# Performance work log

Hardware: AMD Instinct MI355X
Metric: run time of the kernel (lower is better)

## Reference

```python
import jax, jax.numpy as jnp
import numpy as np


def _prelu(x, a):
    return jnp.where(x >= 0, x, a * x)


def _conv1x1(x, w, b, a):
    # x: (B,C,H,W), w: (O,C), b: (O,), a: PReLU scalar (shared, torch default)
    y = jnp.einsum('bchw,oc->bohw', x, w) + b[None, :, None, None]
    return _prelu(y, a)


def setup_inputs() -> dict:
    key = jax.random.key(0)
    ks = jax.random.split(key, 7)
    B, C, H, W = 8, 128, 256, 256
    std = 1.0 / np.sqrt(C)
    x = jax.random.normal(ks[0], (B, C, H, W), dtype=jnp.float32)
    Wf = jax.random.normal(ks[1], (C, C), dtype=jnp.float32) * std
    bf = jax.random.normal(ks[2], (C,), dtype=jnp.float32) * std
    Wg = jax.random.normal(ks[3], (C, C), dtype=jnp.float32) * std
    bg = jax.random.normal(ks[4], (C,), dtype=jnp.float32) * std
    Wh = jax.random.normal(ks[5], (C, C), dtype=jnp.float32) * std
    bh = jax.random.normal(ks[6], (C,), dtype=jnp.float32) * std
    af = jnp.float32(0.25)
    ag = jnp.float32(0.25)
    ah = jnp.float32(0.25)
    return {"x": x, "Wf": Wf, "bf": bf, "af": af,
            "Wg": Wg, "bg": bg, "ag": ag,
            "Wh": Wh, "bh": bh, "ah": ah}


def reference(x, Wf, bf, af, Wg, bg, ag, Wh, bh, ah):
    # 1x1 conv projections + PReLU
    map_f = _conv1x1(x, Wf, bf, af)          # (B,C,H,W)
    map_g = _conv1x1(x, Wg, bg, ag)          # (B,C,H,W)
    map_h = _conv1x1(x, Wh, bh, ah)          # (B,C,H,W)
    # map_f.transpose(2,3) @ map_g -> (B,C,W,W), unscaled single-head attention
    atten = jnp.einsum('bchw,bchv->bcwv', map_f, map_g)  # (B,C,W,W)
    atten = jax.nn.softmax(atten, axis=-1)
    # map_h @ atten -> (B,C,H,W)
    out = jnp.einsum('bchw,bcwv->bchv', map_h, atten)
    return out + x
```

## Files before the change

### kernel.cpp

```cpp
#include <hip/hip_runtime.h>

typedef __bf16 bf16_t;
typedef __bf16 bf16x8 __attribute__((ext_vector_type(8)));
typedef __bf16 bf16x4 __attribute__((ext_vector_type(4)));
typedef float  f32x4  __attribute__((ext_vector_type(4)));

#define HW_ 65536
#define C_  128

__device__ __forceinline__ int swz(int r) { return ((r ^ (r >> 3)) & 7) << 4; }

template<bool HBLK>
__device__ __forceinline__ void conv_one(char* lds, const float* __restrict__ Wsrc,
                                         const float* __restrict__ bias, float alpha,
                                         bf16_t* __restrict__ dst, size_t pb,
                                         int wv, int lr, int lq, int t, int s0)
{
  __syncthreads();
  #pragma unroll
  for (int rep = 0; rep < 16; ++rep) {
    int q = rep * 256 + t;
    int o = q >> 5, c0 = (q & 31) * 4;
    f32x4 w4 = *(const f32x4*)(Wsrc + o * C_ + c0);
    bf16x4 v;
    v[0] = (bf16_t)w4[0]; v[1] = (bf16_t)w4[1]; v[2] = (bf16_t)w4[2]; v[3] = (bf16_t)w4[3];
    *(bf16x4*)(lds + 32768 + ((o * 256 + c0 * 2) ^ swz(o))) = v;
  }
  __syncthreads();

  const f32x4 fz = {0.f, 0.f, 0.f, 0.f};
  f32x4 acc[2][8];
  #pragma unroll
  for (int mf = 0; mf < 2; ++mf)
    #pragma unroll
    for (int nf = 0; nf < 8; ++nf)
      acc[mf][nf] = fz;

  #pragma unroll
  for (int ks = 0; ks < 4; ++ks) {
    int kb = ks * 32 + lq * 8;
    bf16x8 a[2], bb[8];
    #pragma unroll
    for (int mf = 0; mf < 2; ++mf) {
      int m = wv * 32 + mf * 16 + lr;
      a[mf] = *(const bf16x8*)(lds + 32768 + ((m * 256 + kb * 2) ^ swz(m)));
    }
    #pragma unroll
    for (int nf = 0; nf < 8; ++nf) {
      int n = nf * 16 + lr;
      bb[nf] = *(const bf16x8*)(lds + ((n * 256 + kb * 2) ^ swz(n)));
    }
    #pragma unroll
    for (int mf = 0; mf < 2; ++mf)
      #pragma unroll
      for (int nf = 0; nf < 8; ++nf)
        acc[mf][nf] = __builtin_amdgcn_mfma_f32_16x16x32_bf16(a[mf], bb[nf], acc[mf][nf], 0, 0, 0);
  }

  #pragma unroll
  for (int mf = 0; mf < 2; ++mf) {
    #pragma unroll
    for (int i = 0; i < 4; ++i) {
      int o = wv * 32 + mf * 16 + lq * 4 + i;
      float bo = bias[o];
      #pragma unroll
      for (int nf = 0; nf < 8; ++nf) {
        int s = s0 + nf * 16 + lr;
        float v = acc[mf][nf][i] + bo;
        v = (v >= 0.f) ? v : alpha * v;
        size_t off;
        if (HBLK) {
          int h = s >> 8, w = s & 255;
          off = pb + (size_t)o * HW_ + (size_t)(w >> 6) * 16384 + h * 64 + (w & 63);
        } else {
          off = pb + (size_t)o * HW_ + s;
        }
        dst[off] = (bf16_t)v;
      }
    }
  }
}

__global__ __launch_bounds__(256, 2) void conv_kernel(
    const float* __restrict__ x,
    const float* __restrict__ Wf, const float* __restrict__ bfp, const float* __restrict__ afp,
    const float* __restrict__ Wg, const float* __restrict__ bgp, const float* __restrict__ agp,
    const float* __restrict__ Wh, const float* __restrict__ bhp, const float* __restrict__ ahp,
    bf16_t* __restrict__ mF, bf16_t* __restrict__ mG, bf16_t* __restrict__ mH, int b0)
{
  __shared__ __align__(16) char lds[65536];
  const int t = threadIdx.x;
  const int bloc = blockIdx.y;
  const int s0 = blockIdx.x * 128;
  const size_t xbase = ((size_t)(b0 + bloc) * C_) * HW_ + s0;

  #pragma unroll
  for (int rep = 0; rep < 4; ++rep) {
    int q = rep * 256 + t;
    int c0 = (q >> 5) * 4, sl0 = (q & 31) * 4;
    f32x4 r[4];
    #pragma unroll
    for (int i = 0; i < 4; ++i)
      r[i] = *(const f32x4*)(x + xbase + (size_t)(c0 + i) * HW_ + sl0);
    #pragma unroll
    for (int js = 0; js < 4; ++js) {
      int s = sl0 + js;
      bf16x4 v;
      v[0] = (bf16_t)r[0][js]; v[1] = (bf16_t)r[1][js];
      v[2] = (bf16_t)r[2][js]; v[3] = (bf16_t)r[3][js];
      *(bf16x4*)(lds + ((s * 256 + c0 * 2) ^ swz(s))) = v;
    }
  }

  const int wv = t >> 6, lane = t & 63, lr = lane & 15, lq = lane >> 4;
  const size_t pb = (size_t)bloc * C_ * HW_;
  conv_one<false>(lds, Wf, bfp, afp[0], mF, pb, wv, lr, lq, t, s0);
  conv_one<false>(lds, Wg, bgp, agp[0], mG, pb, wv, lr, lq, t, s0);
  conv_one<true >(lds, Wh, bhp, ahp[0], mH, pb, wv, lr, lq, t, s0);
}

#define GT_OFF  32768
#define HS_OFF  131072
#define SMAX_OFF 151552
#define SSUM_OFF 153600
#define SMEM_BYTES 155648

__global__ __launch_bounds__(512, 2) void attn_kernel(
    const bf16_t* __restrict__ mF, const bf16_t* __restrict__ mG, const bf16_t* __restrict__ mH,
    const float* __restrict__ x, float* __restrict__ out, int b0)
{
  extern __shared__ __align__(16) char smem[];
  const int t = threadIdx.x;
  const int c = blockIdx.x, bloc = blockIdx.y;
  const int wv = t >> 6, lane = t & 63, lr = lane & 15, lq = lane >> 4;
  const int wr = wv >> 1, wc = wv & 1;
  const size_t plane  = ((size_t)bloc * C_ + c) * HW_;
  const size_t gplane = (((size_t)(b0 + bloc)) * C_ + c) * HW_;

  const f32x4 fz = {0.f, 0.f, 0.f, 0.f};
  f32x4 acc[4][8];
  #pragma unroll
  for (int mf = 0; mf < 4; ++mf)
    #pragma unroll
    for (int nf = 0; nf < 8; ++nf)
      acc[mf][nf] = fz;

  const int hq = t >> 5, wb8 = t & 31;

  for (int hb = 0; hb < 256; hb += 64) {
    __syncthreads();
    {
      bf16x8 r[4];
      #pragma unroll
      for (int i = 0; i < 4; ++i)
        r[i] = *(const bf16x8*)(mF + plane + (size_t)(hb + hq * 4 + i) * 256 + wb8 * 8);
      #pragma unroll
      for (int j = 0; j < 8; ++j) {
        int w = wb8 * 8 + j;
        bf16x4 v; v[0] = r[0][j]; v[1] = r[1][j]; v[2] = r[2][j]; v[3] = r[3][j];
        *(bf16x4*)(smem + ((w * 128 + hq * 8) ^ swz(w))) = v;
      }
      #pragma unroll
      for (int i = 0; i < 4; ++i)
        r[i] = *(const bf16x8*)(mG + plane + (size_t)(hb + hq * 4 + i) * 256 + wb8 * 8);
      #pragma unroll
      for (int j = 0; j < 8; ++j) {
        int w = wb8 * 8 + j;
        bf16x4 v; v[0] = r[0][j]; v[1] = r[1][j]; v[2] = r[2][j]; v[3] = r[3][j];
        *(bf16x4*)(smem + GT_OFF + ((w * 128 + hq * 8) ^ swz(w))) = v;
      }
    }
    __syncthreads();
    #pragma unroll
    for (int k0 = 0; k0 < 64; k0 += 32) {
      int kb = k0 + lq * 8;
      bf16x8 a[4], bb[8];
      #pragma unroll
      for (int mf = 0; mf < 4; ++mf) {
        int m = wr * 64 + mf * 16 + lr;
        a[mf] = *(const bf16x8*)(smem + ((m * 128 + kb * 2) ^ swz(m)));
      }
      #pragma unroll
      for (int nf = 0; nf < 8; ++nf) {
        int n = wc * 128 + nf * 16 + lr;
        bb[nf] = *(const bf16x8*)(smem + GT_OFF + ((n * 128 + kb * 2) ^ swz(n)));
      }
      #pragma unroll
      for (int mf = 0; mf < 4; ++mf)
        #pragma unroll
        for (int nf = 0; nf < 8; ++nf)
          acc[mf][nf] = __builtin_amdgcn_mfma_f32_16x16x32_bf16(a[mf], bb[nf], acc[mf][nf], 0, 0, 0);
    }
  }

  float* smax = (float*)(smem + SMAX_OFF);
  float* ssum = (float*)(smem + SSUM_OFF);
  float rowm[4][4];
  #pragma unroll
  for (int mf = 0; mf < 4; ++mf)
    #pragma unroll
    for (int i = 0; i < 4; ++i) {
      float m = acc[mf][0][i];
      #pragma unroll
      for (int nf = 1; nf < 8; ++nf) m = fmaxf(m, acc[mf][nf][i]);
      #pragma unroll
      for (int d = 1; d < 16; d <<= 1) m = fmaxf(m, __shfl_xor(m, d));
      rowm[mf][i] = m;
    }
  if (lr == 0) {
    #pragma unroll
    for (int mf = 0; mf < 4; ++mf)
      #pragma unroll
      for (int i = 0; i < 4; ++i)
        smax[wc * 256 + wr * 64 + mf * 16 + lq * 4 + i] = rowm[mf][i];
  }
  __syncthreads();
  float m2[4][4], rs[4][4];
  #pragma unroll
  for (int mf = 0; mf < 4; ++mf)
    #pragma unroll
    for (int i = 0; i < 4; ++i) {
      int w = wr * 64 + mf * 16 + lq * 4 + i;
      m2[mf][i] = fmaxf(smax[w], smax[256 + w]);
      rs[mf][i] = 0.f;
    }
  #pragma unroll
  for (int mf = 0; mf < 4; ++mf)
    #pragma unroll
    for (int nf = 0; nf < 8; ++nf)
      #pragma unroll
      for (int i = 0; i < 4; ++i) {
        float e = __expf(acc[mf][nf][i] - m2[mf][i]);
        acc[mf][nf][i] = e;
        rs[mf][i] += e;
      }
  #pragma unroll
  for (int mf = 0; mf < 4; ++mf)
    #pragma unroll
    for (int i = 0; i < 4; ++i) {
      float s = rs[mf][i];
      #pragma unroll
      for (int d = 1; d < 16; d <<= 1) s += __shfl_xor(s, d);
      rs[mf][i] = s;
    }
  if (lr == 0) {
    #pragma unroll
    for (int mf = 0; mf < 4; ++mf)
      #pragma unroll
      for (int i = 0; i < 4; ++i)
        ssum[wc * 256 + wr * 64 + mf * 16 + lq * 4 + i] = rs[mf][i];
  }
  __syncthreads();
  #pragma unroll
  for (int mf = 0; mf < 4; ++mf)
    #pragma unroll
    for (int i = 0; i < 4; ++i) {
      int w = wr * 64 + mf * 16 + lq * 4 + i;
      float rinv = 1.f / (ssum[w] + ssum[256 + w]);
      #pragma unroll
      for (int nf = 0; nf < 8; ++nf) {
        int v_ = wc * 128 + nf * 16 + lr;
        *(bf16_t*)(smem + ((v_ * 512 + w * 2) ^ swz(v_))) = (bf16_t)(acc[mf][nf][i] * rinv);
      }
    }

  #pragma unroll
  for (int mf = 0; mf < 4; ++mf)
    #pragma unroll
    for (int nf = 0; nf < 8; ++nf)
      acc[mf][nf] = fz;

  for (int wk = 0; wk < 8; ++wk) {
    __syncthreads();
    {
      const size_t hbase = plane + (size_t)(wk >> 1) * 16384 + (size_t)(wk & 1) * 32;
      #pragma unroll
      for (int rep = 0; rep < 2; ++rep) {
        int u = rep * 512 + t;
        int h = u >> 2, wl0 = (u & 3) * 8;
        bf16x8 r = *(const bf16x8*)(mH + hbase + h * 64 + wl0);
        *(bf16x8*)(smem + HS_OFF + h * 80 + wl0 * 2) = r;
      }
    }
    __syncthreads();
    int kb = lq * 8;
    bf16x8 a[4], bb[8];
    #pragma unroll
    for (int mf = 0; mf < 4; ++mf) {
      int m = wr * 64 + mf * 16 + lr;
      a[mf] = *(const bf16x8*)(smem + HS_OFF + m * 80 + kb * 2);
    }
    #pragma unroll
    for (int nf = 0; nf < 8; ++nf) {
      int n = wc * 128 + nf * 16 + lr;
      int kg = wk * 32 + kb;
      bb[nf] = *(const bf16x8*)(smem + ((n * 512 + kg * 2) ^ swz(n)));
    }
    #pragma unroll
    for (int mf = 0; mf < 4; ++mf)
      #pragma unroll
      for (int nf = 0; nf < 8; ++nf)
        acc[mf][nf] = __builtin_amdgcn_mfma_f32_16x16x32_bf16(a[mf], bb[nf], acc[mf][nf], 0, 0, 0);
  }

  #pragma unroll
  for (int mf = 0; mf < 4; ++mf)
    #pragma unroll
    for (int i = 0; i < 4; ++i) {
      int h = wr * 64 + mf * 16 + lq * 4 + i;
      #pragma unroll
      for (int nf = 0; nf < 8; ++nf) {
        int v_ = wc * 128 + nf * 16 + lr;
        size_t off = gplane + (size_t)h * 256 + v_;
        out[off] = acc[mf][nf][i] + x[off];
      }
    }
}

extern "C" void kernel_launch(void* const* d_in, const int* in_sizes, int n_in,
                              void* d_out, int out_size, void* d_ws, size_t ws_size,
                              hipStream_t stream)
{
  (void)in_sizes; (void)n_in; (void)out_size;
  const float* x   = (const float*)d_in[0];
  const float* Wf  = (const float*)d_in[1];
  const float* bfp = (const float*)d_in[2];
  const float* afp = (const float*)d_in[3];
  const float* Wg  = (const float*)d_in[4];
  const float* bgp = (const float*)d_in[5];
  const float* agp = (const float*)d_in[6];
  const float* Wh  = (const float*)d_in[7];
  const float* bhp = (const float*)d_in[8];
  const float* ahp = (const float*)d_in[9];
  float* out = (float*)d_out;

  const size_t per_map_b = (size_t)C_ * HW_ * sizeof(bf16_t);
  int nb = 1;
  if      (ws_size >= 3 * 8 * per_map_b) nb = 8;
  else if (ws_size >= 3 * 4 * per_map_b) nb = 4;
  else if (ws_size >= 3 * 2 * per_map_b) nb = 2;

  hipFuncSetAttribute(reinterpret_cast<const void*>(attn_kernel),
                      hipFuncAttributeMaxDynamicSharedMemorySize, SMEM_BYTES);

  bf16_t* mF = (bf16_t*)d_ws;
  bf16_t* mG = mF + (size_t)nb * C_ * HW_;
  bf16_t* mH = mG + (size_t)nb * C_ * HW_;

  for (int b0 = 0; b0 < 8; b0 += nb) {
    conv_kernel<<<dim3(512, nb), 256, 0, stream>>>(x, Wf, bfp, afp, Wg, bgp, agp,
                                                   Wh, bhp, ahp, mF, mG, mH, b0);
    attn_kernel<<<dim3(C_, nb), 512, SMEM_BYTES, stream>>>(mF, mG, mH, x, out, b0);
  }
}
```

Measured before the change: 403.9 us.

## Rework attention kernel to 1024 threads with register prefetch and direct-global P@V operands

The attention kernel goes from 512 to 1024 threads, with 16 waves laid out 4x4. Each wave now holds 4x4 MFMA tiles instead of 4x8, which lowers accumulator register pressure. In the QK phase, half the threads load F and half load G, and the next 64-row chunk is prefetched into registers while LDS is consumed. The P@V phase no longer stages mH through LDS: H fragments are read straight from global memory into double-buffered registers (aA/aB), so the per-step syncthreads go away and LDS use shrinks. The risks are uncoalesced-ish direct global operand loads and fewer blocks resident per CU at 1024 threads with about 136KB of LDS.

New measurement: 492.5 us. 21.9% more time.

```diff
diff --git a/kernel.cpp b/kernel.cpp
--- a/kernel.cpp
+++ b/kernel.cpp
@@ -119,189 +119,192 @@
   conv_one<true >(lds, Wh, bhp, ahp[0], mH, pb, wv, lr, lq, t, s0);
 }
 
-#define GT_OFF  32768
-#define HS_OFF  131072
-#define SMAX_OFF 151552
-#define SSUM_OFF 153600
-#define SMEM_BYTES 155648
-
-__global__ __launch_bounds__(512, 2) void attn_kernel(
+#define SMAX_OFF 131072
+#define SSUM_OFF 135168
+#define ATTN_SMEM 139264
+
+__global__ __launch_bounds__(1024, 4) void attn_kernel(
     const bf16_t* __restrict__ mF, const bf16_t* __restrict__ mG, const bf16_t* __restrict__ mH,
     const float* __restrict__ x, float* __restrict__ out, int b0)
 {
   extern __shared__ __align__(16) char smem[];
   const int t = threadIdx.x;
   const int c = blockIdx.x, bloc = blockIdx.y;
-  const int wv = t >> 6, lane = t & 63, lr = lane & 15, lq = lane >> 4;
-  const int wr = wv >> 1, wc = wv & 1;
+  const int lane = t & 63, lr = lane & 15, lq = lane >> 4;
+  const int wv = t >> 6, wr = wv >> 2, wc = wv & 3;
   const size_t plane  = ((size_t)bloc * C_ + c) * HW_;
   const size_t gplane = (((size_t)(b0 + bloc)) * C_ + c) * HW_;
 
   const f32x4 fz = {0.f, 0.f, 0.f, 0.f};
-  f32x4 acc[4][8];
+  f32x4 acc[4][4];
   #pragma unroll
   for (int mf = 0; mf < 4; ++mf)
     #pragma unroll
-    for (int nf = 0; nf < 8; ++nf)
+    for (int nf = 0; nf < 4; ++nf)
       acc[mf][nf] = fz;
 
-  const int hq = t >> 5, wb8 = t & 31;
-
-  for (int hb = 0; hb < 256; hb += 64) {
+  const int sg = t >> 9;
+  const int u  = t & 511;
+  const int w0 = (u & 31) * 8, h0 = (u >> 5) * 4;
+  const bf16_t* sp = sg ? mG : mF;
+  char* sd = smem + sg * 32768;
+
+  bf16x8 pf[4];
+  #pragma unroll
+  for (int i = 0; i < 4; ++i)
+    pf[i] = *(const bf16x8*)(sp + plane + (size_t)(h0 + i) * 256 + w0);
+
+  #pragma unroll
+  for (int hc = 0; hc < 4; ++hc) {
+    #pragma unroll
+    for (int j = 0; j < 8; ++j) {
+      int w = w0 + j;
+      bf16x4 v; v[0] = pf[0][j]; v[1] = pf[1][j]; v[2] = pf[2][j]; v[3] = pf[3][j];
+      *(bf16x4*)(sd + ((w * 128 + h0 * 2) ^ swz(w))) = v;
+    }
+    if (hc < 3) {
+      #pragma unroll
+      for (int i = 0; i < 4; ++i)
+        pf[i] = *(const bf16x8*)(sp + plane + (size_t)((hc + 1) * 64 + h0 + i) * 256 + w0);
+    }
     __syncthreads();
-    {
-      bf16x8 r[4];
-      #pragma unroll
-      for (int i = 0; i < 4; ++i)
-        r[i] = *(const bf16x8*)(mF + plane + (size_t)(hb + hq * 4 + i) * 256 + wb8 * 8);
-      #pragma unroll
-      for (int j = 0; j < 8; ++j) {
-        int w = wb8 * 8 + j;
-        bf16x4 v; v[0] = r[0][j]; v[1] = r[1][j]; v[2] = r[2][j]; v[3] = r[3][j];
-        *(bf16x4*)(smem + ((w * 128 + hq * 8) ^ swz(w))) = v;
-      }
-      #pragma unroll
-      for (int i = 0; i < 4; ++i)
-        r[i] = *(const bf16x8*)(mG + plane + (size_t)(hb + hq * 4 + i) * 256 + wb8 * 8);
-      #pragma unroll
-      for (int j = 0; j < 8; ++j) {
-        int w = wb8 * 8 + j;
-        bf16x4 v; v[0] = r[0][j]; v[1] = r[1][j]; v[2] = r[2][j]; v[3] = r[3][j];
-        *(bf16x4*)(smem + GT_OFF + ((w * 128 + hq * 8) ^ swz(w))) = v;
-      }
-    }
-    __syncthreads();
     #pragma unroll
     for (int k0 = 0; k0 < 64; k0 += 32) {
-      int kb = k0 + lq * 8;
-      bf16x8 a[4], bb[8];
+      const int kb = k0 + lq * 8;
+      bf16x8 af[4], bq[4];
       #pragma unroll
       for (int mf = 0; mf < 4; ++mf) {
         int m = wr * 64 + mf * 16 + lr;
-        a[mf] = *(const bf16x8*)(smem + ((m * 128 + kb * 2) ^ swz(m)));
-      }
-      #pragma unroll
-      for (int nf = 0; nf < 8; ++nf) {
-        int n = wc * 128 + nf * 16 + lr;
-        bb[nf] = *(const bf16x8*)(smem + GT_OFF + ((n * 128 + kb * 2) ^ swz(n)));
+        af[mf] = *(const bf16x8*)(smem + ((m * 128 + kb * 2) ^ swz(m)));
+      }
+      #pragma unroll
+      for (int nf = 0; nf < 4; ++nf) {
+        int n = wc * 64 + nf * 16 + lr;
+        bq[nf] = *(const bf16x8*)(smem + 32768 + ((n * 128 + kb * 2) ^ swz(n)));
       }
       #pragma unroll
       for (int mf = 0; mf < 4; ++mf)
         #pragma unroll
-        for (int nf = 0; nf < 8; ++nf)
-          acc[mf][nf] = __builtin_amdgcn_mfma_f32_16x16x32_bf16(a[mf], bb[nf], acc[mf][nf], 0, 0, 0);
-    }
+        for (int nf = 0; nf < 4; ++nf)
+          acc[mf][nf] = __builtin_amdgcn_mfma_f32_16x16x32_bf16(af[mf], bq[nf], acc[mf][nf], 0, 0, 0);
+    }
+    __syncthreads();
   }
 
   float* smax = (float*)(smem + SMAX_OFF);
   float* ssum = (float*)(smem + SSUM_OFF);
-  float rowm[4][4];
+  float rinv[4][4];
+  {
+    float rowm[4][4];
+    #pragma unroll
+    for (int mf = 0; mf < 4; ++mf)
+      #pragma unroll
+      for (int i = 0; i < 4; ++i) {
+        float m = fmaxf(fmaxf(acc[mf][0][i], acc[mf][1][i]),
+                        fmaxf(acc[mf][2][i], acc[mf][3][i]));
+        #pragma unroll
+        for (int d = 1; d < 16; d <<= 1) m = fmaxf(m, __shfl_xor(m, d));
+        rowm[mf][i] = m;
+      }
+    if (lr == 0) {
+      #pragma unroll
+      for (int mf = 0; mf < 4; ++mf)
+        #pragma unroll
+        for (int i = 0; i < 4; ++i)
+          smax[wc * 256 + wr * 64 + mf * 16 + lq * 4 + i] = rowm[mf][i];
+    }
+    __syncthreads();
+    #pragma unroll
+    for (int mf = 0; mf < 4; ++mf)
+      #pragma unroll
+      for (int i = 0; i < 4; ++i) {
+        int w = wr * 64 + mf * 16 + lq * 4 + i;
+        rowm[mf][i] = fmaxf(fmaxf(smax[w], smax[256 + w]),
+                            fmaxf(smax[512 + w], smax[768 + w]));
+      }
+    #pragma unroll
+    for (int mf = 0; mf < 4; ++mf)
+      #pragma unroll
+      for (int i = 0; i < 4; ++i) {
+        float rs = 0.f;
+        #pragma unroll
+        for (int nf = 0; nf < 4; ++nf) {
+          float e = __expf(acc[mf][nf][i] - rowm[mf][i]);
+          acc[mf][nf][i] = e;
+          rs += e;
+        }
+        #pragma unroll
+        for (int d = 1; d < 16; d <<= 1) rs += __shfl_xor(rs, d);
+        if (lr == 0) ssum[wc * 256 + wr * 64 + mf * 16 + lq * 4 + i] = rs;
+      }
+    __syncthreads();
+    #pragma unroll
+    for (int mf = 0; mf < 4; ++mf)
+      #pragma unroll
+      for (int i = 0; i < 4; ++i) {
+        int w = wr * 64 + mf * 16 + lq * 4 + i;
+        rinv[mf][i] = 1.f / (ssum[w] + ssum[256 + w] + ssum[512 + w] + ssum[768 + w]);
+      }
+  }
+
+  bf16x8 aA[4], aB[4];
+  #pragma unroll
+  for (int mf = 0; mf < 4; ++mf) {
+    int h = wr * 64 + mf * 16 + lr;
+    aA[mf] = *(const bf16x8*)(mH + plane + (size_t)h * 64 + lq * 8);
+  }
+
+  #pragma unroll
+  for (int mf = 0; mf < 4; ++mf) {
+    int wpb = (wr * 64 + mf * 16 + lq * 4) * 2;
+    #pragma unroll
+    for (int nf = 0; nf < 4; ++nf) {
+      int v_ = wc * 64 + nf * 16 + lr;
+      bf16x4 v;
+      #pragma unroll
+      for (int i = 0; i < 4; ++i) v[i] = (bf16_t)(acc[mf][nf][i] * rinv[mf][i]);
+      *(bf16x4*)(smem + ((v_ * 512 + wpb) ^ swz(v_))) = v;
+    }
+  }
+  #pragma unroll
+  for (int mf = 0; mf < 4; ++mf) {
+    int h = wr * 64 + mf * 16 + lr;
+    aB[mf] = *(const bf16x8*)(mH + plane + (size_t)h * 64 + 32 + lq * 8);
+  }
+
   #pragma unroll
   for (int mf = 0; mf < 4; ++mf)
     #pragma unroll
-    for (int i = 0; i < 4; ++i) {
-      float m = acc[mf][0][i];
-      #pragma unroll
-      for (int nf = 1; nf < 8; ++nf) m = fmaxf(m, acc[mf][nf][i]);
-      #pragma unroll
-      for (int d = 1; d < 16; d <<= 1) m = fmaxf(m, __shfl_xor(m, d));
-      rowm[mf][i] = m;
-    }
-  if (lr == 0) {
-    #pragma unroll
-    for (int mf = 0; mf < 4; ++mf)
-      #pragma unroll
-      for (int i = 0; i < 4; ++i)
-        smax[wc * 256 + wr * 64 + mf * 16 + lq * 4 + i] = rowm[mf][i];
-  }
+    for (int nf = 0; nf < 4; ++nf)
+      acc[mf][nf] = fz;
   __syncthreads();
-  float m2[4][4], rs[4][4];
-  #pragma unroll
-  for (int mf = 0; mf < 4; ++mf)
-    #pragma unroll
-    for (int i = 0; i < 4; ++i) {
-      int w = wr * 64 + mf * 16 + lq * 4 + i;
-      m2[mf][i] = fmaxf(smax[w], smax[256 + w]);
-      rs[mf][i] = 0.f;
-    }
-  #pragma unroll
-  for (int mf = 0; mf < 4; ++mf)
-    #pragma unroll
-    for (int nf = 0; nf < 8; ++nf)
-      #pragma unroll
-      for (int i = 0; i < 4; ++i) {
-        float e = __expf(acc[mf][nf][i] - m2[mf][i]);
-        acc[mf][nf][i] = e;
-        rs[mf][i] += e;
-      }
-  #pragma unroll
-  for (int mf = 0; mf < 4; ++mf)
-    #pragma unroll
-    for (int i = 0; i < 4; ++i) {
-      float s = rs[mf][i];
-      #pragma unroll
-      for (int d = 1; d < 16; d <<= 1) s += __shfl_xor(s, d);
-      rs[mf][i] = s;
-    }
-  if (lr == 0) {
-    #pragma unroll
-    for (int mf = 0; mf < 4; ++mf)
-      #pragma unroll
-      for (int i = 0; i < 4; ++i)
-        ssum[wc * 256 + wr * 64 + mf * 16 + lq * 4 + i] = rs[mf][i];
-  }
-  __syncthreads();
-  #pragma unroll
-  for (int mf = 0; mf < 4; ++mf)
-    #pragma unroll
-    for (int i = 0; i < 4; ++i) {
-      int w = wr * 64 + mf * 16 + lq * 4 + i;
-      float rinv = 1.f / (ssum[w] + ssum[256 + w]);
-      #pragma unroll
-      for (int nf = 0; nf < 8; ++nf) {
-        int v_ = wc * 128 + nf * 16 + lr;
-        *(bf16_t*)(smem + ((v_ * 512 + w * 2) ^ swz(v_))) = (bf16_t)(acc[mf][nf][i] * rinv);
-      }
-    }
-
-  #pragma unroll
-  for (int mf = 0; mf < 4; ++mf)
-    #pragma unroll
-    for (int nf = 0; nf < 8; ++nf)
-      acc[mf][nf] = fz;
-
-  for (int wk = 0; wk < 8; ++wk) {
-    __syncthreads();
-    {
-      const size_t hbase = plane + (size_t)(wk >> 1) * 16384 + (size_t)(wk & 1) * 32;
-      #pragma unroll
-      for (int rep = 0; rep < 2; ++rep) {
-        int u = rep * 512 + t;
-        int h = u >> 2, wl0 = (u & 3) * 8;
-        bf16x8 r = *(const bf16x8*)(mH + hbase + h * 64 + wl0);
-        *(bf16x8*)(smem + HS_OFF + h * 80 + wl0 * 2) = r;
-      }
-    }
-    __syncthreads();
-    int kb = lq * 8;
-    bf16x8 a[4], bb[8];
-    #pragma unroll
-    for (int mf = 0; mf < 4; ++mf) {
-      int m = wr * 64 + mf * 16 + lr;
-      a[mf] = *(const bf16x8*)(smem + HS_OFF + m * 80 + kb * 2);
-    }
-    #pragma unroll
-    for (int nf = 0; nf < 8; ++nf) {
-      int n = wc * 128 + nf * 16 + lr;
-      int kg = wk * 32 + kb;
-      bb[nf] = *(const bf16x8*)(smem + ((n * 512 + kg * 2) ^ swz(n)));
-    }
-    #pragma unroll
-    for (int mf = 0; mf < 4; ++mf)
-      #pragma unroll
-      for (int nf = 0; nf < 8; ++nf)
-        acc[mf][nf] = __builtin_amdgcn_mfma_f32_16x16x32_bf16(a[mf], bb[nf], acc[mf][nf], 0, 0, 0);
-  }
+
+#define PV_STEP(KS, AC)                                                          \
+  {                                                                              \
+    bf16x8 bq[4];                                                                \
+    _Pragma("unroll")                                                            \
+    for (int nf = 0; nf < 4; ++nf) {                                             \
+      int v_ = wc * 64 + nf * 16 + lr;                                           \
+      bq[nf] = *(const bf16x8*)(smem + ((v_ * 512 + (KS) * 64 + lq * 16) ^ swz(v_))); \
+    }                                                                            \
+    _Pragma("unroll")                                                            \
+    for (int mf = 0; mf < 4; ++mf)                                               \
+      _Pragma("unroll")                                                          \
+      for (int nf = 0; nf < 4; ++nf)                                             \
+        acc[mf][nf] = __builtin_amdgcn_mfma_f32_16x16x32_bf16(AC[mf], bq[nf], acc[mf][nf], 0, 0, 0); \
+    if ((KS) < 6) {                                                              \
+      _Pragma("unroll")                                                          \
+      for (int mf = 0; mf < 4; ++mf) {                                           \
+        int h = wr * 64 + mf * 16 + lr;                                          \
+        AC[mf] = *(const bf16x8*)(mH + plane + (size_t)(((KS) + 2) >> 1) * 16384 \
+                                  + (size_t)h * 64 + (((KS) + 2) & 1) * 32 + lq * 8); \
+      }                                                                          \
+    }                                                                            \
+  }
+
+  PV_STEP(0, aA) PV_STEP(1, aB) PV_STEP(2, aA) PV_STEP(3, aB)
+  PV_STEP(4, aA) PV_STEP(5, aB) PV_STEP(6, aA) PV_STEP(7, aB)
+#undef PV_STEP
 
   #pragma unroll
   for (int mf = 0; mf < 4; ++mf)
@@ -309,8 +312,8 @@
     for (int i = 0; i < 4; ++i) {
       int h = wr * 64 + mf * 16 + lq * 4 + i;
       #pragma unroll
-      for (int nf = 0; nf < 8; ++nf) {
-        int v_ = wc * 128 + nf * 16 + lr;
+      for (int nf = 0; nf < 4; ++nf) {
+        int v_ = wc * 64 + nf * 16 + lr;
         size_t off = gplane + (size_t)h * 256 + v_;
         out[off] = acc[mf][nf][i] + x[off];
       }
@@ -341,7 +344,7 @@
   else if (ws_size >= 3 * 2 * per_map_b) nb = 2;
 
   hipFuncSetAttribute(reinterpret_cast<const void*>(attn_kernel),
-                      hipFuncAttributeMaxDynamicSharedMemorySize, SMEM_BYTES);
+                      hipFuncAttributeMaxDynamicSharedMemorySize, ATTN_SMEM);
 
   bf16_t* mF = (bf16_t*)d_ws;
   bf16_t* mG = mF + (size_t)nb * C_ * HW_;
@@ -350,6 +353,6 @@
   for (int b0 = 0; b0 < 8; b0 += nb) {
     conv_kernel<<<dim3(512, nb), 256, 0, stream>>>(x, Wf, bfp, afp, Wg, bgp, agp,
                                                    Wh, bhp, ahp, mF, mG, mH, b0);
-    attn_kernel<<<dim3(C_, nb), 512, SMEM_BYTES, stream>>>(mF, mG, mH, x, out, b0);
+    attn_kernel<<<dim3(C_, nb), 1024, ATTN_SMEM, stream>>>(mF, mG, mH, x, out, b0);
   }
 }
```

## Prefetch F/G tiles in registers and stream H directly into MFMA operands

Applied to the files above, without the earlier changes.

The attention kernel now prefetches the next 64-row F/G tile into registers while the current tile is in LDS, using lighter raw barriers instead of two __syncthreads per step. The second GEMM no longer stages H through LDS. The conv kernel writes H in 32-column blocks so each wave can load its A fragments straight from global memory through a 3-deep register ring, and each wave now covers 32 rows by all 256 columns. Shared memory drops, which could raise occupancy, but register pressure grows (32 accumulators plus prefetch buffers), and the custom barriers depend on correct waitcnt handling.

Result: slower. 434.5 us (+7.6%).

```diff
diff --git a/kernel.cpp b/kernel.cpp
--- a/kernel.cpp
+++ b/kernel.cpp
@@ -9,6 +9,13 @@
 #define C_  128
 
 __device__ __forceinline__ int swz(int r) { return ((r ^ (r >> 3)) & 7) << 4; }
+
+#define LGKM0() asm volatile("s_waitcnt lgkmcnt(0)" ::: "memory")
+__device__ __forceinline__ void BAR() {
+  asm volatile("" ::: "memory");
+  __builtin_amdgcn_s_barrier();
+  asm volatile("" ::: "memory");
+}
 
 template<bool HBLK>
 __device__ __forceinline__ void conv_one(char* lds, const float* __restrict__ Wsrc,
@@ -71,7 +78,7 @@
         size_t off;
         if (HBLK) {
           int h = s >> 8, w = s & 255;
-          off = pb + (size_t)o * HW_ + (size_t)(w >> 6) * 16384 + h * 64 + (w & 63);
+          off = pb + (size_t)o * HW_ + (size_t)(w >> 5) * 8192 + h * 32 + (w & 31);
         } else {
           off = pb + (size_t)o * HW_ + s;
         }
@@ -119,11 +126,9 @@
   conv_one<true >(lds, Wh, bhp, ahp[0], mH, pb, wv, lr, lq, t, s0);
 }
 
-#define GT_OFF  32768
-#define HS_OFF  131072
-#define SMAX_OFF 151552
-#define SSUM_OFF 153600
-#define SMEM_BYTES 155648
+#define SMAX_OFF 131072
+#define SSUM_OFF 133120
+#define ATTN_SMEM 135168
 
 __global__ __launch_bounds__(512, 2) void attn_kernel(
     const bf16_t* __restrict__ mF, const bf16_t* __restrict__ mG, const bf16_t* __restrict__ mH,
@@ -132,8 +137,8 @@
   extern __shared__ __align__(16) char smem[];
   const int t = threadIdx.x;
   const int c = blockIdx.x, bloc = blockIdx.y;
-  const int wv = t >> 6, lane = t & 63, lr = lane & 15, lq = lane >> 4;
-  const int wr = wv >> 1, wc = wv & 1;
+  const int lane = t & 63, lr = lane & 15, lq = lane >> 4;
+  const int wv = t >> 6, wr = wv >> 1, wc = wv & 1;
   const size_t plane  = ((size_t)bloc * C_ + c) * HW_;
   const size_t gplane = (((size_t)(b0 + bloc)) * C_ + c) * HW_;
 
@@ -147,50 +152,52 @@
 
   const int hq = t >> 5, wb8 = t & 31;
 
+  bf16x8 pfF[4], pfG[4];
+  #pragma unroll
+  for (int i = 0; i < 4; ++i) {
+    pfF[i] = *(const bf16x8*)(mF + plane + (size_t)(hq * 4 + i) * 256 + wb8 * 8);
+    pfG[i] = *(const bf16x8*)(mG + plane + (size_t)(hq * 4 + i) * 256 + wb8 * 8);
+  }
+
+  #pragma unroll
   for (int hb = 0; hb < 256; hb += 64) {
-    __syncthreads();
-    {
-      bf16x8 r[4];
-      #pragma unroll
-      for (int i = 0; i < 4; ++i)
-        r[i] = *(const bf16x8*)(mF + plane + (size_t)(hb + hq * 4 + i) * 256 + wb8 * 8);
-      #pragma unroll
-      for (int j = 0; j < 8; ++j) {
-        int w = wb8 * 8 + j;
-        bf16x4 v; v[0] = r[0][j]; v[1] = r[1][j]; v[2] = r[2][j]; v[3] = r[3][j];
-        *(bf16x4*)(smem + ((w * 128 + hq * 8) ^ swz(w))) = v;
-      }
-      #pragma unroll
-      for (int i = 0; i < 4; ++i)
-        r[i] = *(const bf16x8*)(mG + plane + (size_t)(hb + hq * 4 + i) * 256 + wb8 * 8);
-      #pragma unroll
-      for (int j = 0; j < 8; ++j) {
-        int w = wb8 * 8 + j;
-        bf16x4 v; v[0] = r[0][j]; v[1] = r[1][j]; v[2] = r[2][j]; v[3] = r[3][j];
-        *(bf16x4*)(smem + GT_OFF + ((w * 128 + hq * 8) ^ swz(w))) = v;
-      }
-    }
-    __syncthreads();
+    #pragma unroll
+    for (int j = 0; j < 8; ++j) {
+      int w = wb8 * 8 + j;
+      bf16x4 v; v[0] = pfF[0][j]; v[1] = pfF[1][j]; v[2] = pfF[2][j]; v[3] = pfF[3][j];
+      *(bf16x4*)(smem + ((w * 128 + hq * 8) ^ swz(w))) = v;
+      bf16x4 g; g[0] = pfG[0][j]; g[1] = pfG[1][j]; g[2] = pfG[2][j]; g[3] = pfG[3][j];
+      *(bf16x4*)(smem + 32768 + ((w * 128 + hq * 8) ^ swz(w))) = g;
+    }
+    if (hb < 192) {
+      #pragma unroll
+      for (int i = 0; i < 4; ++i) {
+        pfF[i] = *(const bf16x8*)(mF + plane + (size_t)(hb + 64 + hq * 4 + i) * 256 + wb8 * 8);
+        pfG[i] = *(const bf16x8*)(mG + plane + (size_t)(hb + 64 + hq * 4 + i) * 256 + wb8 * 8);
+      }
+    }
+    LGKM0(); BAR();
     #pragma unroll
     for (int k0 = 0; k0 < 64; k0 += 32) {
-      int kb = k0 + lq * 8;
-      bf16x8 a[4], bb[8];
+      const int kb = k0 + lq * 8;
+      bf16x8 af[4], bq[8];
       #pragma unroll
       for (int mf = 0; mf < 4; ++mf) {
         int m = wr * 64 + mf * 16 + lr;
-        a[mf] = *(const bf16x8*)(smem + ((m * 128 + kb * 2) ^ swz(m)));
+        af[mf] = *(const bf16x8*)(smem + ((m * 128 + kb * 2) ^ swz(m)));
       }
       #pragma unroll
       for (int nf = 0; nf < 8; ++nf) {
         int n = wc * 128 + nf * 16 + lr;
-        bb[nf] = *(const bf16x8*)(smem + GT_OFF + ((n * 128 + kb * 2) ^ swz(n)));
+        bq[nf] = *(const bf16x8*)(smem + 32768 + ((n * 128 + kb * 2) ^ swz(n)));
       }
       #pragma unroll
       for (int mf = 0; mf < 4; ++mf)
         #pragma unroll
         for (int nf = 0; nf < 8; ++nf)
-          acc[mf][nf] = __builtin_amdgcn_mfma_f32_16x16x32_bf16(a[mf], bb[nf], acc[mf][nf], 0, 0, 0);
-    }
+          acc[mf][nf] = __builtin_amdgcn_mfma_f32_16x16x32_bf16(af[mf], bq[nf], acc[mf][nf], 0, 0, 0);
+    }
+    BAR();
   }
 
   float* smax = (float*)(smem + SMAX_OFF);
@@ -214,7 +221,7 @@
       for (int i = 0; i < 4; ++i)
         smax[wc * 256 + wr * 64 + mf * 16 + lq * 4 + i] = rowm[mf][i];
   }
-  __syncthreads();
+  LGKM0(); BAR();
   float m2[4][4], rs[4][4];
   #pragma unroll
   for (int mf = 0; mf < 4; ++mf)
@@ -250,69 +257,77 @@
       for (int i = 0; i < 4; ++i)
         ssum[wc * 256 + wr * 64 + mf * 16 + lq * 4 + i] = rs[mf][i];
   }
-  __syncthreads();
-  #pragma unroll
-  for (int mf = 0; mf < 4; ++mf)
+  LGKM0(); BAR();
+
+  #pragma unroll
+  for (int mf = 0; mf < 4; ++mf) {
+    float rinv[4];
     #pragma unroll
     for (int i = 0; i < 4; ++i) {
       int w = wr * 64 + mf * 16 + lq * 4 + i;
-      float rinv = 1.f / (ssum[w] + ssum[256 + w]);
-      #pragma unroll
-      for (int nf = 0; nf < 8; ++nf) {
-        int v_ = wc * 128 + nf * 16 + lr;
-        *(bf16_t*)(smem + ((v_ * 512 + w * 2) ^ swz(v_))) = (bf16_t)(acc[mf][nf][i] * rinv);
-      }
-    }
-
-  #pragma unroll
-  for (int mf = 0; mf < 4; ++mf)
-    #pragma unroll
-    for (int nf = 0; nf < 8; ++nf)
-      acc[mf][nf] = fz;
-
-  for (int wk = 0; wk < 8; ++wk) {
-    __syncthreads();
-    {
-      const size_t hbase = plane + (size_t)(wk >> 1) * 16384 + (size_t)(wk & 1) * 32;
-      #pragma unroll
-      for (int rep = 0; rep < 2; ++rep) {
-        int u = rep * 512 + t;
-        int h = u >> 2, wl0 = (u & 3) * 8;
-        bf16x8 r = *(const bf16x8*)(mH + hbase + h * 64 + wl0);
-        *(bf16x8*)(smem + HS_OFF + h * 80 + wl0 * 2) = r;
-      }
-    }
-    __syncthreads();
-    int kb = lq * 8;
-    bf16x8 a[4], bb[8];
-    #pragma unroll
-    for (int mf = 0; mf < 4; ++mf) {
-      int m = wr * 64 + mf * 16 + lr;
-      a[mf] = *(const bf16x8*)(smem + HS_OFF + m * 80 + kb * 2);
-    }
+      rinv[i] = 1.f / (ssum[w] + ssum[256 + w]);
+    }
+    int wpb = (wr * 64 + mf * 16 + lq * 4) * 2;
     #pragma unroll
     for (int nf = 0; nf < 8; ++nf) {
-      int n = wc * 128 + nf * 16 + lr;
-      int kg = wk * 32 + kb;
-      bb[nf] = *(const bf16x8*)(smem + ((n * 512 + kg * 2) ^ swz(n)));
-    }
-    #pragma unroll
-    for (int mf = 0; mf < 4; ++mf)
-      #pragma unroll
-      for (int nf = 0; nf < 8; ++nf)
-        acc[mf][nf] = __builtin_amdgcn_mfma_f32_16x16x32_bf16(a[mf], bb[nf], acc[mf][nf], 0, 0, 0);
-  }
-
-  #pragma unroll
-  for (int mf = 0; mf < 4; ++mf)
-    #pragma unroll
-    for (int i = 0; i < 4; ++i) {
-      int h = wr * 64 + mf * 16 + lq * 4 + i;
-      #pragma unroll
-      for (int nf = 0; nf < 8; ++nf) {
-        int v_ = wc * 128 + nf * 16 + lr;
+      int v_ = wc * 128 + nf * 16 + lr;
+      bf16x4 v;
+      #pragma unroll
+      for (int i = 0; i < 4; ++i) v[i] = (bf16_t)(acc[mf][nf][i] * rinv[i]);
+      *(bf16x4*)(smem + ((v_ * 512 + wpb) ^ swz(v_))) = v;
+    }
+  }
+
+  const bf16_t* hp = mH + plane;
+  bf16x8 aP[3][2];
+  #pragma unroll
+  for (int p = 0; p < 3; ++p)
+    #pragma unroll
+    for (int mf = 0; mf < 2; ++mf) {
+      int h = wv * 32 + mf * 16 + lr;
+      aP[p][mf] = *(const bf16x8*)(hp + (size_t)p * 8192 + h * 32 + lq * 8);
+    }
+
+  LGKM0(); BAR();
+
+  f32x4 oac[2][16];
+  #pragma unroll
+  for (int mf = 0; mf < 2; ++mf)
+    #pragma unroll
+    for (int nf = 0; nf < 16; ++nf)
+      oac[mf][nf] = fz;
+
+  __builtin_amdgcn_s_setprio(1);
+  #pragma unroll
+  for (int kc = 0; kc < 8; ++kc) {
+    bf16x8 a0 = aP[kc % 3][0], a1 = aP[kc % 3][1];
+    if (kc < 5) {
+      #pragma unroll
+      for (int mf = 0; mf < 2; ++mf) {
+        int h = wv * 32 + mf * 16 + lr;
+        aP[kc % 3][mf] = *(const bf16x8*)(hp + (size_t)(kc + 3) * 8192 + h * 32 + lq * 8);
+      }
+    }
+    #pragma unroll
+    for (int nf = 0; nf < 16; ++nf) {
+      int v_ = nf * 16 + lr;
+      bf16x8 bq = *(const bf16x8*)(smem + ((v_ * 512 + kc * 64 + lq * 16) ^ swz(v_)));
+      oac[0][nf] = __builtin_amdgcn_mfma_f32_16x16x32_bf16(a0, bq, oac[0][nf], 0, 0, 0);
+      oac[1][nf] = __builtin_amdgcn_mfma_f32_16x16x32_bf16(a1, bq, oac[1][nf], 0, 0, 0);
+    }
+  }
+  __builtin_amdgcn_s_setprio(0);
+
+  #pragma unroll
+  for (int mf = 0; mf < 2; ++mf)
+    #pragma unroll
+    for (int i = 0; i < 4; ++i) {
+      int h = wv * 32 + mf * 16 + lq * 4 + i;
+      #pragma unroll
+      for (int nf = 0; nf < 16; ++nf) {
+        int v_ = nf * 16 + lr;
         size_t off = gplane + (size_t)h * 256 + v_;
-        out[off] = acc[mf][nf][i] + x[off];
+        out[off] = oac[mf][nf][i] + x[off];
       }
     }
 }
@@ -341,7 +356,7 @@
   else if (ws_size >= 3 * 2 * per_map_b) nb = 2;
 
   hipFuncSetAttribute(reinterpret_cast<const void*>(attn_kernel),
-                      hipFuncAttributeMaxDynamicSharedMemorySize, SMEM_BYTES);
+                      hipFuncAttributeMaxDynamicSharedMemorySize, ATTN_SMEM);
 
   bf16_t* mF = (bf16_t*)d_ws;
   bf16_t* mG = mF + (size_t)nb * C_ * HW_;
@@ -350,6 +365,6 @@
   for (int b0 = 0; b0 < 8; b0 += nb) {
     conv_kernel<<<dim3(512, nb), 256, 0, stream>>>(x, Wf, bfp, afp, Wg, bgp, agp,
                                                    Wh, bhp, ahp, mF, mG, mH, b0);
-    attn_kernel<<<dim3(C_, nb), 512, SMEM_BYTES, stream>>>(mF, mG, mH, x, out, b0);
-  }
-}
+    attn_kernel<<<dim3(C_, nb), 512, ATTN_SMEM, stream>>>(mF, mG, mH, x, out, b0);
+  }
+}
```
